# Kernel tuning notes

Hardware: AMD Instinct MI355X
Metric: run time of the kernel (lower is better)

The kernel has to match this reference:

```python
import math
import jax, jax.numpy as jnp
import numpy as np

D_MODEL = 1024
HEAD_DIM = 64  # D_MODEL // NUM_HEADS
B, T = 8, 2048


def setup_inputs() -> dict:
    key = jax.random.key(0)
    k1, k2, k3, k4 = jax.random.split(key, 4)
    x = jax.random.normal(k1, (B, T, D_MODEL), dtype=jnp.float32)
    wq = jax.random.normal(k2, (D_MODEL, HEAD_DIM), dtype=jnp.float32) * (1.0 / math.sqrt(D_MODEL))
    wk = jax.random.normal(k3, (D_MODEL, HEAD_DIM), dtype=jnp.float32) * (1.0 / math.sqrt(D_MODEL))
    wv = jax.random.normal(k4, (D_MODEL, HEAD_DIM), dtype=jnp.float32) * (1.0 / math.sqrt(D_MODEL))
    return {"x": x, "wq": wq, "wk": wk, "wv": wv}


def reference(x, wq, wk, wv):
    # Single-head causal scaled dot-product attention (dropout = eval/identity).
    Tn = x.shape[1]
    q = jnp.einsum('btc,ch->bth', x, wq)  # [B,T,H]
    k = jnp.einsum('btc,ch->bth', x, wk)
    v = jnp.einsum('btc,ch->bth', x, wv)
    scale = 1.0 / math.sqrt(HEAD_DIM)
    scores = jnp.einsum('bth,bsh->bts', q, k) * scale  # [B,T,T]
    causal = jnp.tril(jnp.ones((Tn, Tn), dtype=bool))
    scores = jnp.where(causal, scores, -jnp.inf)
    weights = jax.nn.softmax(scores, axis=-1)
    return jnp.einsum('bts,bsh->bth', weights, v)  # [B,T,H]
```

## Files before the change

### kernel.cpp

```cpp
#include <hip/hip_runtime.h>

#define D_MODEL 1024
#define HDIM    64
#define BATCH   8
#define SEQ     2048
#define BT      (BATCH*SEQ)
#define NCAT    192
#define KSTEP   32
#define NKS     (D_MODEL/KSTEP)
#define FRAGSH  512
#define STEPSH  (24*FRAGSH)

typedef __attribute__((ext_vector_type(8))) short s8v;
typedef __attribute__((ext_vector_type(4))) float f4;

__device__ __forceinline__ unsigned short f2bf(float f){
    unsigned u = __builtin_bit_cast(unsigned, f);
    u += 0x7fffu + ((u >> 16) & 1u);
    return (unsigned short)(u >> 16);
}
__device__ __forceinline__ float bf2f(unsigned short h){
    unsigned u = ((unsigned)h) << 16;
    return __builtin_bit_cast(float, u);
}
__device__ __forceinline__ f4 MFMA(s8v a, s8v b, f4 c){
    return __builtin_amdgcn_mfma_f32_16x16x32_bf16(a, b, c, 0, 0, 0);
}

__global__ void prep_w_kernel(const float* __restrict__ wq, const float* __restrict__ wk,
                              const float* __restrict__ wv,
                              short* __restrict__ wtP){
    int ncat = blockIdx.x;
    const float* w = (ncat < 64) ? wq : ((ncat < 128) ? wk : wv);
    int n  = ncat & 63;
    int nb = ncat >> 4, ln = ncat & 15;
    for (int k = threadIdx.x; k < D_MODEL; k += blockDim.x){
        float f = w[k*HDIM + n];
        unsigned short h = f2bf(f);
        unsigned short l = f2bf(f - bf2f(h));
        int t1 = k >> 5, g = (k >> 3) & 3, e = k & 7;
        size_t base = (size_t)t1*STEPSH + (size_t)((g*16 + ln) << 3) + e;
        wtP[base + (size_t)nb*FRAGSH]        = (short)h;
        wtP[base + (size_t)(12 + nb)*FRAGSH] = (short)l;
    }
}

__global__ __launch_bounds__(256) void proj_kernel(
        const float* __restrict__ x,
        const short* __restrict__ wtP,
        short* __restrict__ q, short* __restrict__ k,
        short* __restrict__ vt){
    __shared__ __align__(16) float xs[4][32][32];
    int tid = threadIdx.x;
    int wid = tid >> 6, lane = tid & 63, g = lane >> 4, ln = lane & 15;
    int m0 = blockIdx.x * 32;

    int sr = tid >> 3, ss = tid & 7;
    const float* xsrc = x + (size_t)(m0 + sr)*D_MODEL + ((ss ^ (sr & 7)) << 2);
    const short* wb   = wtP + (size_t)(wid*3)*FRAGSH + (size_t)lane*8;

    f4 acc[6];
#pragma unroll
    for (int i = 0; i < 6; i++) acc[i] = (f4){0.f,0.f,0.f,0.f};

    s8v whA0, whA1, whA2, wlA0, wlA1, wlA2;
    s8v whB0, whB1, whB2, wlB0, wlB1, wlB2;

#define GLOADX(T) { \
    __builtin_amdgcn_global_load_lds(xsrc + (size_t)(T)*KSTEP, \
                                     &xs[(T) & 3][wid*8][0], 16, 0, 0); }

#define LOADW(P, T) { \
    const short* wp = wb + (size_t)(T)*STEPSH; \
    wh##P##0 = *(const s8v*)(wp); \
    wh##P##1 = *(const s8v*)(wp + FRAGSH); \
    wh##P##2 = *(const s8v*)(wp + 2*FRAGSH); \
    wl##P##0 = *(const s8v*)(wp + 12*FRAGSH); \
    wl##P##1 = *(const s8v*)(wp + 13*FRAGSH); \
    wl##P##2 = *(const s8v*)(wp + 14*FRAGSH); }

#define CVT8(DST, VA, VB) { \
    DST[0] = (short)f2bf(VA.x); DST[1] = (short)f2bf(VA.y); \
    DST[2] = (short)f2bf(VA.z); DST[3] = (short)f2bf(VA.w); \
    DST[4] = (short)f2bf(VB.x); DST[5] = (short)f2bf(VB.y); \
    DST[6] = (short)f2bf(VB.z); DST[7] = (short)f2bf(VB.w); }

#define MFMAS(P, A0, A1) { \
    acc[0] = MFMA(A0, wh##P##0, acc[0]); acc[0] = MFMA(A0, wl##P##0, acc[0]); \
    acc[1] = MFMA(A0, wh##P##1, acc[1]); acc[1] = MFMA(A0, wl##P##1, acc[1]); \
    acc[2] = MFMA(A0, wh##P##2, acc[2]); acc[2] = MFMA(A0, wl##P##2, acc[2]); \
    acc[3] = MFMA(A1, wh##P##0, acc[3]); acc[3] = MFMA(A1, wl##P##0, acc[3]); \
    acc[4] = MFMA(A1, wh##P##1, acc[4]); acc[4] = MFMA(A1, wl##P##1, acc[4]); \
    acc[5] = MFMA(A1, wh##P##2, acc[5]); acc[5] = MFMA(A1, wl##P##2, acc[5]); }

#define STEP(P, T, VM) { \
    asm volatile("s_waitcnt vmcnt(" #VM ")" ::: "memory"); \
    __builtin_amdgcn_s_barrier(); \
    __builtin_amdgcn_sched_barrier(0); \
    int bq = (T) & 3, r7 = ln & 7; \
    float4 xa = *(const float4*)&xs[bq][ln]     [((2*g)   ^ r7) << 2]; \
    float4 xb = *(const float4*)&xs[bq][ln]     [((2*g+1) ^ r7) << 2]; \
    float4 xc = *(const float4*)&xs[bq][ln + 16][((2*g)   ^ r7) << 2]; \
    float4 xd = *(const float4*)&xs[bq][ln + 16][((2*g+1) ^ r7) << 2]; \
    s8v A0, A1; \
    CVT8(A0, xa, xb) \
    CVT8(A1, xc, xd) \
    MFMAS(P, A0, A1) \
    if ((T) + 2 < NKS) LOADW(P, (T) + 2) \
    __builtin_amdgcn_sched_barrier(0); \
    if ((T) + 3 < NKS) GLOADX((T) + 3) \
    __builtin_amdgcn_sched_barrier(0); \
}

    GLOADX(0)
    GLOADX(1)
    GLOADX(2)
    __builtin_amdgcn_sched_barrier(0);
    LOADW(A, 0)
    LOADW(B, 1)

    for (int t = 0; t < 30; t += 2){
        STEP(A, t,     14)
        STEP(B, t + 1, 14)
    }
    STEP(A, 30, 13)
    STEP(B, 31, 6)
#undef GLOADX
#undef LOADW
#undef CVT8
#undef MFMAS
#undef STEP

#pragma unroll
    for (int rf = 0; rf < 2; rf++){
#pragma unroll
        for (int nb = 0; nb < 3; nb++){
            int ncat = wid*48 + nb*16 + ln;
            int mat = ncat >> 6, h = ncat & 63;
#pragma unroll
            for (int r = 0; r < 4; r++){
                size_t trow = (size_t)m0 + rf*16 + g*4 + r;
                float v = acc[rf*3 + nb][r];
                unsigned short hh = f2bf(v);
                if (mat == 0){
                    q[trow*HDIM + h] = (short)hh;
                } else if (mat == 1){
                    k[trow*HDIM + h] = (short)hh;
                } else {
                    size_t bb = trow >> 11, t2 = trow & 2047;
                    vt[((bb*HDIM + h) << 11) + t2] = (short)hh;
                }
            }
        }
    }
}

__global__ __launch_bounds__(256, 5) void attn_kernel(
        const short* __restrict__ qg, const short* __restrict__ kg,
        const short* __restrict__ vt, float* __restrict__ out){
    __shared__ unsigned short plds[4][16][112];
    __shared__ float olds[4][16][65];
    __shared__ float mlds[4][16], llds[4][16];
    const float SC = 0.125f * 1.44269504088896340736f;
    int tid = threadIdx.x;
    int w = tid >> 6, lane = tid & 63, g = lane >> 4, ln = lane & 15;
    int b = blockIdx.y;
    int qi = ((blockIdx.y >> 1) & 1) ? (int)(gridDim.x - 1 - blockIdx.x) : (int)blockIdx.x;
    int tq = qi * 16;

    size_t qoff = ((size_t)b*SEQ + tq + ln) * HDIM + g*8;
    s8v q0 = *(const s8v*)(qg + qoff);
    s8v q1 = *(const s8v*)(qg + qoff + 32);

    f4 o0 = {0.f,0.f,0.f,0.f}, o1 = o0, o2 = o0, o3 = o0;
    float m[4], lsum[4];
#pragma unroll
    for (int r = 0; r < 4; r++){ m[r] = -__builtin_inff(); lsum[r] = 0.f; }

    int ntiles = (tq + 79) >> 6;
    for (int ti = w; ti < ntiles; ti += 4){
        int s0 = ti << 6;
        size_t kbase = ((size_t)b*SEQ + s0 + ln) * HDIM + g*8;
        f4 z0, z1, z2, z3;
#define QK_SUBTILE(ZJ, J) { \
        const short* kp = kg + kbase + (J)*16*HDIM; \
        s8v k0 = *(const s8v*)(kp); \
        s8v k1 = *(const s8v*)(kp + 32); \
        f4 s = {0.f,0.f,0.f,0.f}; \
        s = MFMA(q0, k0, s); s = MFMA(q1, k1, s); \
        ZJ[0] = s[0]*SC; ZJ[1] = s[1]*SC; ZJ[2] = s[2]*SC; ZJ[3] = s[3]*SC; }
        QK_SUBTILE(z0, 0)
        QK_SUBTILE(z1, 1)
        QK_SUBTILE(z2, 2)
        QK_SUBTILE(z3, 3)
#undef QK_SUBTILE
        if (s0 + 63 > tq){
#pragma unroll
            for (int r = 0; r < 4; r++){
                int t = tq + g*4 + r;
                if (s0      + ln > t) z0[r] = -__builtin_inff();
                if (s0 + 16 + ln > t) z1[r] = -__builtin_inff();
                if (s0 + 32 + ln > t) z2[r] = -__builtin_inff();
                if (s0 + 48 + ln > t) z3[r] = -__builtin_inff();
            }
        }
        float al[4];
#pragma unroll
        for (int r = 0; r < 4; r++){
            float v = fmaxf(fmaxf(z0[r], z1[r]), fmaxf(z2[r], z3[r]));
            v = fmaxf(v, __shfl_xor(v, 1));
            v = fmaxf(v, __shfl_xor(v, 2));
            v = fmaxf(v, __shfl_xor(v, 4));
            v = fmaxf(v, __shfl_xor(v, 8));
            float mn = fmaxf(m[r], v);
            al[r] = __builtin_amdgcn_exp2f(m[r] - mn);
            float p0 = __builtin_amdgcn_exp2f(z0[r] - mn);
            float p1 = __builtin_amdgcn_exp2f(z1[r] - mn);
            float p2 = __builtin_amdgcn_exp2f(z2[r] - mn);
            float p3 = __builtin_amdgcn_exp2f(z3[r] - mn);
            lsum[r] = lsum[r]*al[r] + ((p0 + p1) + (p2 + p3));
            m[r] = mn;
            int row = g*4 + r;
            plds[w][row][ln]      = f2bf(p0);
            plds[w][row][ln + 16] = f2bf(p1);
            plds[w][row][ln + 32] = f2bf(p2);
            plds[w][row][ln + 48] = f2bf(p3);
        }
#pragma unroll
        for (int r = 0; r < 4; r++){
            o0[r] *= al[r]; o1[r] *= al[r]; o2[r] *= al[r]; o3[r] *= al[r];
        }
        asm volatile("s_waitcnt lgkmcnt(0)" ::: "memory");
        __builtin_amdgcn_sched_barrier(0);
        s8v pa0 = *(const s8v*)&plds[w][ln][g*8];
        s8v pa1 = *(const s8v*)&plds[w][ln][32 + g*8];
        size_t voff = ((size_t)b*HDIM + ln) * SEQ + s0 + g*8;
        s8v v00 = *(const s8v*)(vt + voff);
        s8v v01 = *(const s8v*)(vt + voff + 32);
        s8v v10 = *(const s8v*)(vt + voff + 16*SEQ);
        s8v v11 = *(const s8v*)(vt + voff + 16*SEQ + 32);
        s8v v20 = *(const s8v*)(vt + voff + 32*SEQ);
        s8v v21 = *(const s8v*)(vt + voff + 32*SEQ + 32);
        s8v v30 = *(const s8v*)(vt + voff + 48*SEQ);
        s8v v31 = *(const s8v*)(vt + voff + 48*SEQ + 32);
        o0 = MFMA(pa0, v00, o0); o0 = MFMA(pa1, v01, o0);
        o1 = MFMA(pa0, v10, o1); o1 = MFMA(pa1, v11, o1);
        o2 = MFMA(pa0, v20, o2); o2 = MFMA(pa1, v21, o2);
        o3 = MFMA(pa0, v30, o3); o3 = MFMA(pa1, v31, o3);
    }

#pragma unroll
    for (int r = 0; r < 4; r++){
        float s = lsum[r];
        s += __shfl_xor(s, 1);
        s += __shfl_xor(s, 2);
        s += __shfl_xor(s, 4);
        s += __shfl_xor(s, 8);
        lsum[r] = s;
    }

#pragma unroll
    for (int r = 0; r < 4; r++){
        int row = g*4 + r;
        olds[w][row][ln]      = o0[r];
        olds[w][row][ln + 16] = o1[r];
        olds[w][row][ln + 32] = o2[r];
        olds[w][row][ln + 48] = o3[r];
        if (ln == 0){ mlds[w][row] = m[r]; llds[w][row] = lsum[r]; }
    }
    __syncthreads();

    {
        int row = tid >> 4;
        int hb  = tid & 15;
        float m0 = mlds[0][row], m1 = mlds[1][row], m2 = mlds[2][row], m3 = mlds[3][row];
        float M = fmaxf(fmaxf(m0, m1), fmaxf(m2, m3));
        float w0 = __builtin_amdgcn_exp2f(m0 - M);
        float w1 = __builtin_amdgcn_exp2f(m1 - M);
        float w2 = __builtin_amdgcn_exp2f(m2 - M);
        float w3 = __builtin_amdgcn_exp2f(m3 - M);
        float L = llds[0][row]*w0 + llds[1][row]*w1 + llds[2][row]*w2 + llds[3][row]*w3;
        float inv = 1.0f / L;
        size_t obase = ((size_t)b*SEQ + tq + row) * HDIM + hb;
#pragma unroll
        for (int j = 0; j < 4; j++){
            int h = hb + 16*j;
            float acc = olds[0][row][h]*w0 + olds[1][row][h]*w1
                      + olds[2][row][h]*w2 + olds[3][row][h]*w3;
            out[obase + 16*j] = acc * inv;
        }
    }
}

extern "C" void kernel_launch(void* const* d_in, const int* in_sizes, int n_in,
                              void* d_out, int out_size, void* d_ws, size_t ws_size,
                              hipStream_t stream) {
    (void)in_sizes; (void)n_in; (void)out_size; (void)ws_size;
    const float* x  = (const float*)d_in[0];
    const float* wq = (const float*)d_in[1];
    const float* wk = (const float*)d_in[2];
    const float* wv = (const float*)d_in[3];
    float* out = (float*)d_out;

    short* ws  = (short*)d_ws;
    short* wtP = ws;
    short* q   = wtP + (size_t)NKS*STEPSH;
    short* k   = q + (size_t)BT*HDIM;
    short* vt  = k + (size_t)BT*HDIM;

    prep_w_kernel<<<NCAT, 256, 0, stream>>>(wq, wk, wv, wtP);
    proj_kernel<<<BT/32, 256, 0, stream>>>(x, wtP, q, k, vt);
    attn_kernel<<<dim3(SEQ/16, BATCH), 256, 0, stream>>>(q, k, vt, out);
}
```

Measured before the change: 68.89 us.

## Drop bf16 hi/lo weight split and enlarge projection tile to 64x64

The weight prep now stores a single bf16 copy instead of a high/low split, which halves the MFMA count in the projection GEMM. The projection kernel is retiled to 64-row blocks with 512 threads, a 64-wide K step and 16 pipeline steps, and each wave now covers a 32-row by 48-column sub-tile. This reduces MFMA work and the number of barrier-synchronised steps, at the cost of lower weight precision, which may hurt accuracy against the fp32 reference, and fewer blocks per launch.

```diff
diff --git a/kernel.cpp b/kernel.cpp
--- a/kernel.cpp
+++ b/kernel.cpp
@@ -6,10 +6,11 @@
 #define SEQ     2048
 #define BT      (BATCH*SEQ)
 #define NCAT    192
-#define KSTEP   32
-#define NKS     (D_MODEL/KSTEP)
-#define FRAGSH  512
-#define STEPSH  (24*FRAGSH)
+#define BM      64
+#define BK      64
+#define NSTEP   16
+#define WFRAG   512
+#define WSTEP32 (12*WFRAG)
 
 typedef __attribute__((ext_vector_type(8))) short s8v;
 typedef __attribute__((ext_vector_type(4))) float f4;
@@ -36,48 +37,53 @@
     int nb = ncat >> 4, ln = ncat & 15;
     for (int k = threadIdx.x; k < D_MODEL; k += blockDim.x){
         float f = w[k*HDIM + n];
-        unsigned short h = f2bf(f);
-        unsigned short l = f2bf(f - bf2f(h));
         int t1 = k >> 5, g = (k >> 3) & 3, e = k & 7;
-        size_t base = (size_t)t1*STEPSH + (size_t)((g*16 + ln) << 3) + e;
-        wtP[base + (size_t)nb*FRAGSH]        = (short)h;
-        wtP[base + (size_t)(12 + nb)*FRAGSH] = (short)l;
-    }
-}
-
-__global__ __launch_bounds__(256) void proj_kernel(
+        wtP[(size_t)t1*WSTEP32 + (size_t)nb*WFRAG + ((g*16 + ln) << 3) + e]
+            = (short)f2bf(f);
+    }
+}
+
+__global__ __launch_bounds__(512) void proj_kernel(
         const float* __restrict__ x,
         const short* __restrict__ wtP,
         short* __restrict__ q, short* __restrict__ k,
         short* __restrict__ vt){
-    __shared__ __align__(16) float xs[4][32][32];
+    __shared__ __align__(16) float xs[4][64][64];
     int tid = threadIdx.x;
     int wid = tid >> 6, lane = tid & 63, g = lane >> 4, ln = lane & 15;
-    int m0 = blockIdx.x * 32;
-
-    int sr = tid >> 3, ss = tid & 7;
-    const float* xsrc = x + (size_t)(m0 + sr)*D_MODEL + ((ss ^ (sr & 7)) << 2);
-    const short* wb   = wtP + (size_t)(wid*3)*FRAGSH + (size_t)lane*8;
+    int wm = wid >> 2, wn = wid & 3;
+    int m0 = blockIdx.x * BM;
+
+    int rowA = wid*8 + (lane >> 4);
+    int rowB = rowA + 4;
+    int sl   = lane & 15;
+    int swzA = (sl & 8) | ((sl & 7) ^ (rowA & 7));
+    int swzB = (sl & 8) | ((sl & 7) ^ (rowB & 7));
+    const float* xsrcA = x + (size_t)(m0 + rowA)*D_MODEL + swzA*4;
+    const float* xsrcB = x + (size_t)(m0 + rowB)*D_MODEL + swzB*4;
+    const short* wb    = wtP + (size_t)(wn*3)*WFRAG + (size_t)lane*8;
 
     f4 acc[6];
 #pragma unroll
     for (int i = 0; i < 6; i++) acc[i] = (f4){0.f,0.f,0.f,0.f};
 
-    s8v whA0, whA1, whA2, wlA0, wlA1, wlA2;
-    s8v whB0, whB1, whB2, wlB0, wlB1, wlB2;
+    s8v wA0, wA1, wA2, wA3, wA4, wA5;
+    s8v wB0, wB1, wB2, wB3, wB4, wB5;
 
 #define GLOADX(T) { \
-    __builtin_amdgcn_global_load_lds(xsrc + (size_t)(T)*KSTEP, \
-                                     &xs[(T) & 3][wid*8][0], 16, 0, 0); }
+    __builtin_amdgcn_global_load_lds(xsrcA + (size_t)(T)*BK, \
+                                     &xs[(T) & 3][wid*8][0], 16, 0, 0); \
+    __builtin_amdgcn_global_load_lds(xsrcB + (size_t)(T)*BK, \
+                                     &xs[(T) & 3][wid*8 + 4][0], 16, 0, 0); }
 
 #define LOADW(P, T) { \
-    const short* wp = wb + (size_t)(T)*STEPSH; \
-    wh##P##0 = *(const s8v*)(wp); \
-    wh##P##1 = *(const s8v*)(wp + FRAGSH); \
-    wh##P##2 = *(const s8v*)(wp + 2*FRAGSH); \
-    wl##P##0 = *(const s8v*)(wp + 12*FRAGSH); \
-    wl##P##1 = *(const s8v*)(wp + 13*FRAGSH); \
-    wl##P##2 = *(const s8v*)(wp + 14*FRAGSH); }
+    const short* wp = wb + (size_t)(2*(T))*WSTEP32; \
+    w##P##0 = *(const s8v*)(wp); \
+    w##P##1 = *(const s8v*)(wp + WFRAG); \
+    w##P##2 = *(const s8v*)(wp + 2*WFRAG); \
+    w##P##3 = *(const s8v*)(wp + WSTEP32); \
+    w##P##4 = *(const s8v*)(wp + WSTEP32 + WFRAG); \
+    w##P##5 = *(const s8v*)(wp + WSTEP32 + 2*WFRAG); }
 
 #define CVT8(DST, VA, VB) { \
     DST[0] = (short)f2bf(VA.x); DST[1] = (short)f2bf(VA.y); \
@@ -85,61 +91,73 @@
     DST[4] = (short)f2bf(VB.x); DST[5] = (short)f2bf(VB.y); \
     DST[6] = (short)f2bf(VB.z); DST[7] = (short)f2bf(VB.w); }
 
-#define MFMAS(P, A0, A1) { \
-    acc[0] = MFMA(A0, wh##P##0, acc[0]); acc[0] = MFMA(A0, wl##P##0, acc[0]); \
-    acc[1] = MFMA(A0, wh##P##1, acc[1]); acc[1] = MFMA(A0, wl##P##1, acc[1]); \
-    acc[2] = MFMA(A0, wh##P##2, acc[2]); acc[2] = MFMA(A0, wl##P##2, acc[2]); \
-    acc[3] = MFMA(A1, wh##P##0, acc[3]); acc[3] = MFMA(A1, wl##P##0, acc[3]); \
-    acc[4] = MFMA(A1, wh##P##1, acc[4]); acc[4] = MFMA(A1, wl##P##1, acc[4]); \
-    acc[5] = MFMA(A1, wh##P##2, acc[5]); acc[5] = MFMA(A1, wl##P##2, acc[5]); }
-
 #define STEP(P, T, VM) { \
     asm volatile("s_waitcnt vmcnt(" #VM ")" ::: "memory"); \
     __builtin_amdgcn_s_barrier(); \
     __builtin_amdgcn_sched_barrier(0); \
     int bq = (T) & 3, r7 = ln & 7; \
-    float4 xa = *(const float4*)&xs[bq][ln]     [((2*g)   ^ r7) << 2]; \
-    float4 xb = *(const float4*)&xs[bq][ln]     [((2*g+1) ^ r7) << 2]; \
-    float4 xc = *(const float4*)&xs[bq][ln + 16][((2*g)   ^ r7) << 2]; \
-    float4 xd = *(const float4*)&xs[bq][ln + 16][((2*g+1) ^ r7) << 2]; \
-    s8v A0, A1; \
-    CVT8(A0, xa, xb) \
-    CVT8(A1, xc, xd) \
-    MFMAS(P, A0, A1) \
-    if ((T) + 2 < NKS) LOADW(P, (T) + 2) \
+    int r0 = wm*32 + ln, r1 = r0 + 16; \
+    float4 xa = *(const float4*)&xs[bq][r0][(((2*g)   ^ r7)) << 2]; \
+    float4 xb = *(const float4*)&xs[bq][r0][(((2*g+1) ^ r7)) << 2]; \
+    float4 xc = *(const float4*)&xs[bq][r1][(((2*g)   ^ r7)) << 2]; \
+    float4 xd = *(const float4*)&xs[bq][r1][(((2*g+1) ^ r7)) << 2]; \
+    float4 xe = *(const float4*)&xs[bq][r0][((8 | ((2*g)   ^ r7))) << 2]; \
+    float4 xf = *(const float4*)&xs[bq][r0][((8 | ((2*g+1) ^ r7))) << 2]; \
+    float4 xg = *(const float4*)&xs[bq][r1][((8 | ((2*g)   ^ r7))) << 2]; \
+    float4 xh = *(const float4*)&xs[bq][r1][((8 | ((2*g+1) ^ r7))) << 2]; \
+    s8v A00, A10, A01, A11; \
+    CVT8(A00, xa, xb) \
+    CVT8(A10, xc, xd) \
+    CVT8(A01, xe, xf) \
+    CVT8(A11, xg, xh) \
+    acc[0] = MFMA(A00, w##P##0, acc[0]); \
+    acc[1] = MFMA(A00, w##P##1, acc[1]); \
+    acc[2] = MFMA(A00, w##P##2, acc[2]); \
+    acc[3] = MFMA(A10, w##P##0, acc[3]); \
+    acc[4] = MFMA(A10, w##P##1, acc[4]); \
+    acc[5] = MFMA(A10, w##P##2, acc[5]); \
+    acc[0] = MFMA(A01, w##P##3, acc[0]); \
+    acc[1] = MFMA(A01, w##P##4, acc[1]); \
+    acc[2] = MFMA(A01, w##P##5, acc[2]); \
+    acc[3] = MFMA(A11, w##P##3, acc[3]); \
+    acc[4] = MFMA(A11, w##P##4, acc[4]); \
+    acc[5] = MFMA(A11, w##P##5, acc[5]); \
     __builtin_amdgcn_sched_barrier(0); \
-    if ((T) + 3 < NKS) GLOADX((T) + 3) \
+    if ((T) + 2 < NSTEP) LOADW(P, (T) + 2) \
     __builtin_amdgcn_sched_barrier(0); \
-}
-
+    if ((T) + 2 < NSTEP) GLOADX((T) + 2) \
+    __builtin_amdgcn_sched_barrier(0); \
+}
+
+    LOADW(A, 0)
+    __builtin_amdgcn_sched_barrier(0);
     GLOADX(0)
+    __builtin_amdgcn_sched_barrier(0);
+    LOADW(B, 1)
+    __builtin_amdgcn_sched_barrier(0);
     GLOADX(1)
-    GLOADX(2)
     __builtin_amdgcn_sched_barrier(0);
-    LOADW(A, 0)
-    LOADW(B, 1)
-
-    for (int t = 0; t < 30; t += 2){
-        STEP(A, t,     14)
-        STEP(B, t + 1, 14)
-    }
-    STEP(A, 30, 13)
-    STEP(B, 31, 6)
+
+    for (int t = 0; t < 14; t += 2){
+        STEP(A, t,     8)
+        STEP(B, t + 1, 8)
+    }
+    STEP(A, 14, 8)
+    STEP(B, 15, 0)
 #undef GLOADX
 #undef LOADW
 #undef CVT8
-#undef MFMAS
 #undef STEP
 
 #pragma unroll
     for (int rf = 0; rf < 2; rf++){
 #pragma unroll
         for (int nb = 0; nb < 3; nb++){
-            int ncat = wid*48 + nb*16 + ln;
+            int ncat = wn*48 + nb*16 + ln;
             int mat = ncat >> 6, h = ncat & 63;
 #pragma unroll
             for (int r = 0; r < 4; r++){
-                size_t trow = (size_t)m0 + rf*16 + g*4 + r;
+                size_t trow = (size_t)m0 + wm*32 + rf*16 + g*4 + r;
                 float v = acc[rf*3 + nb][r];
                 unsigned short hh = f2bf(v);
                 if (mat == 0){
@@ -304,11 +322,11 @@
 
     short* ws  = (short*)d_ws;
     short* wtP = ws;
-    short* q   = wtP + (size_t)NKS*STEPSH;
+    short* q   = wtP + (size_t)32*WSTEP32;
     short* k   = q + (size_t)BT*HDIM;
     short* vt  = k + (size_t)BT*HDIM;
 
     prep_w_kernel<<<NCAT, 256, 0, stream>>>(wq, wk, wv, wtP);
-    proj_kernel<<<BT/32, 256, 0, stream>>>(x, wtP, q, k, vt);
+    proj_kernel<<<BT/BM, 512, 0, stream>>>(x, wtP, q, k, vt);
     attn_kernel<<<dim3(SEQ/16, BATCH), 256, 0, stream>>>(q, k, vt, out);
 }
```

Result: faster. 61.26 us (-11.1%).
